# Kernel optimization log

Measured on AMD Instinct MI355X. Metric: run time of the kernel, lower is better.

The kernel has to match this reference:

```python
import jax, jax.numpy as jnp
import numpy as np

T, B, I, H = 256, 32, 128, 256
CLIP = 2.0

def setup_inputs() -> dict:
    key = jax.random.key(0)
    ks = jax.random.split(key, 10)
    si, sh = 1.0 / np.sqrt(I), 1.0 / np.sqrt(H)
    return {
        "x":     jax.random.normal(ks[0], (T, B, I), jnp.float32),
        "Wx":    jax.random.normal(ks[1], (4 * H, I), jnp.float32) * si,
        "bx":    jax.random.normal(ks[2], (4 * H,), jnp.float32) * si,
        "Wh":    jax.random.normal(ks[3], (4 * H, H), jnp.float32) * sh,
        "bh":    jax.random.normal(ks[4], (4 * H,), jnp.float32) * sh,
        "w_mod": jax.random.normal(ks[5], (1, H), jnp.float32) * sh,
        "b_mod": jax.random.normal(ks[6], (1,), jnp.float32) * sh,
        "w_fan": jax.random.normal(ks[7], (H, 1), jnp.float32),
        "b_fan": jax.random.normal(ks[8], (H,), jnp.float32),
        "alpha": 1e-4 * jax.random.uniform(ks[9], (H, H), jnp.float32),
    }

def reference(x, Wx, bx, Wh, bh, w_mod, b_mod, w_fan, b_fan, alpha):
    Bn = x.shape[1]
    # precompute input projection for all timesteps: [T, B, 4H]
    xf = jnp.einsum('tbi,gi->tbg', x, Wx) + bx

    def step(state, xf_t):
        h, c, hebb = state  # h,c: [B,H]; hebb: [B,H,H]
        fioj = xf_t + h @ Wh.T + bh                     # [B,4H]
        f = jax.nn.sigmoid(fioj[:, :H])
        i = jax.nn.sigmoid(fioj[:, H:2 * H])
        o = jax.nn.sigmoid(fioj[:, 2 * H:3 * H])
        # h_pred @ (alpha * hebb) : batched vec-mat product
        plast = jnp.einsum('bh,hk,bhk->bk', h, alpha, hebb)
        j = jnp.tanh(fioj[:, 3 * H:] + plast)
        c_new = f * c + i * j
        h_new = o * jnp.tanh(c_new)
        eta = jnp.tanh(c_new @ w_mod.T + b_mod)          # [B,1]
        myeta = eta * w_fan[:, 0] + b_fan                # [B,H] (Linear(1,H) fanout)
        # delta_hebb = outer(h_pred, j); eta modulates along the j axis
        hebb_new = jnp.clip(hebb + myeta[:, None, :] * (h[:, :, None] * j[:, None, :]),
                            -CLIP, CLIP)
        return (h_new, c_new, hebb_new), h_new

    init = (jnp.zeros((Bn, H), jnp.float32),
            jnp.zeros((Bn, H), jnp.float32),
            jnp.zeros((Bn, H, H), jnp.float32))
    (h, c, hebb), hs = jax.lax.scan(step, init, xf)
    return hs, h, c, hebb
```

## Files before the change

### kernel.cpp

```cpp
#include <hip/hip_runtime.h>


#define TT 256
#define BB 32
#define II 128
#define HH 256
#define G4 1024

typedef _Float16 h2_t __attribute__((ext_vector_type(2)));
typedef unsigned long long u64;

__device__ __forceinline__ float sigm(float x) {
    return 1.0f / (1.0f + __expf(-x));
}
__device__ __forceinline__ float tanhfast(float x) {
    return 1.0f - 2.0f / (__expf(2.0f * x) + 1.0f);
}
__device__ __forceinline__ unsigned pkh(float lo, float hi) {
    h2_t v;
    v.x = (_Float16)lo;
    v.y = (_Float16)hi;
    return __builtin_bit_cast(unsigned, v);
}

#if __has_builtin(__builtin_amdgcn_fdot2)
__device__ __forceinline__ float dot2(unsigned a, unsigned b, float c) {
    return __builtin_amdgcn_fdot2(__builtin_bit_cast(h2_t, a),
                                  __builtin_bit_cast(h2_t, b), c, false);
}
#else
__device__ __forceinline__ float dot2(unsigned a, unsigned b, float c) {
    h2_t av = __builtin_bit_cast(h2_t, a), bv = __builtin_bit_cast(h2_t, b);
    return c + (float)av.x * (float)bv.x + (float)av.y * (float)bv.y;
}
#endif

__device__ __forceinline__ h2_t pkfma(h2_t a, h2_t b, h2_t c) {
#if __has_builtin(__builtin_elementwise_fma)
    return __builtin_elementwise_fma(a, b, c);
#else
    return a * b + c;
#endif
}
__device__ __forceinline__ h2_t clip2h(h2_t x) {
    const h2_t lo = {(_Float16)-2.0f, (_Float16)-2.0f};
    const h2_t hi = {(_Float16)2.0f, (_Float16)2.0f};
#if __has_builtin(__builtin_elementwise_max) && __has_builtin(__builtin_elementwise_min)
    return __builtin_elementwise_min(__builtin_elementwise_max(x, lo), hi);
#else
    h2_t r = x;
    r.x = r.x < lo.x ? lo.x : (r.x > hi.x ? hi.x : r.x);
    r.y = r.y < lo.y ? lo.y : (r.y > hi.y ? hi.y : r.y);
    return r;
#endif
}

__device__ __forceinline__ void ld3_fast(const u64* p1, const u64* p2,
                                         const u64* p3,
                                         u64& v1, u64& v2, u64& v3) {
    asm volatile(
        "global_load_dwordx2 %0, %3, off sc0\n\t"
        "global_load_dwordx2 %1, %4, off sc0\n\t"
        "global_load_dwordx2 %2, %5, off sc0\n\t"
        "s_waitcnt vmcnt(0)"
        : "=&v"(v1), "=&v"(v2), "=&v"(v3)
        : "v"(p1), "v"(p2), "v"(p3));
}

__global__ __launch_bounds__(256) void prep_wd3(const float* __restrict__ Wh,
                                                uint4* __restrict__ Wd3) {
    int idx = blockIdx.x * 256 + threadIdx.x;
    int ro = idx >> 12, rem = idx & 4095;
    int g = rem >> 2, ri = rem & 3;
    int r8 = 4 * ro + ri;
    const float4* s = (const float4*)(Wh + (size_t)g * HH + (r8 << 3));
    float4 a = s[0], b2 = s[1];
    uint4 o;
    o.x = pkh(a.x, a.y);
    o.y = pkh(a.z, a.w);
    o.z = pkh(b2.x, b2.y);
    o.w = pkh(b2.z, b2.w);
    Wd3[idx] = o;
}

__global__ __launch_bounds__(256) void prep_alq(const float* __restrict__ alpha,
                                                uint4* __restrict__ alQ) {
    int idx = blockIdx.x * 256 + threadIdx.x;
    int p4 = idx >> 8, k = idx & 255;
    unsigned r[4];
#pragma unroll
    for (int j = 0; j < 4; ++j) {
        int p = 4 * p4 + j;
        float a0 = alpha[(size_t)(2 * p) * HH + k];
        float a1 = alpha[(size_t)(2 * p + 1) * HH + k];
        r[j] = pkh(a0, a1);
    }
    uint4 o; o.x = r[0]; o.y = r[1]; o.z = r[2]; o.w = r[3];
    alQ[idx] = o;
}

__global__ __launch_bounds__(256) void xf_gemm(const float* __restrict__ x,
                                               const float* __restrict__ Wx,
                                               const float* __restrict__ bx,
                                               const float* __restrict__ bh,
                                               float* __restrict__ xf) {
    __shared__ float As[64][37];
    __shared__ float Bs[64][37];
    const int tid = threadIdx.x;
    const int tx = tid & 15, ty = tid >> 4;
    const int m0 = blockIdx.y << 6;
    const int n0 = blockIdx.x << 6;
    float c[4][4] = {};

    for (int k0 = 0; k0 < II; k0 += 32) {
#pragma unroll
        for (int hh = 0; hh < 2; ++hh) {
            int row = (tid >> 3) + (hh << 5);
            int col = (tid & 7) << 2;
            float4 va = *(const float4*)(x + (size_t)(m0 + row) * II + k0 + col);
            As[row][col] = va.x; As[row][col + 1] = va.y;
            As[row][col + 2] = va.z; As[row][col + 3] = va.w;
            float4 vb = *(const float4*)(Wx + (size_t)(n0 + row) * II + k0 + col);
            Bs[row][col] = vb.x; Bs[row][col + 1] = vb.y;
            Bs[row][col + 2] = vb.z; Bs[row][col + 3] = vb.w;
        }
        __syncthreads();
#pragma unroll
        for (int kk = 0; kk < 32; ++kk) {
            float a[4], bb[4];
#pragma unroll
            for (int u = 0; u < 4; ++u) a[u] = As[(ty << 2) + u][kk];
#pragma unroll
            for (int v = 0; v < 4; ++v) bb[v] = Bs[(tx << 2) + v][kk];
#pragma unroll
            for (int u = 0; u < 4; ++u)
#pragma unroll
                for (int v = 0; v < 4; ++v)
                    c[u][v] = fmaf(a[u], bb[v], c[u][v]);
        }
        __syncthreads();
    }
    const int n = n0 + (tx << 2);
    float4 bxv = *(const float4*)(bx + n);
    float4 bhv = *(const float4*)(bh + n);
    float4 badd = {bxv.x + bhv.x, bxv.y + bhv.y, bxv.z + bhv.z, bxv.w + bhv.w};
#pragma unroll
    for (int u = 0; u < 4; ++u) {
        int m = m0 + (ty << 2) + u;
        float4 o = {c[u][0] + badd.x, c[u][1] + badd.y,
                    c[u][2] + badd.z, c[u][3] + badd.w};
        *(float4*)(xf + (size_t)m * G4 + n) = o;
    }
}

#define HBQ_FOREACH(X) X(0) X(1) X(2) X(3) X(4) X(5) X(6) X(7)

#define HBQ_DECL(i) h2_t hp##i = {(_Float16)0.0f, (_Float16)0.0f};
#define HBQ_OUT(i) \
    hbout[(size_t)(r0g + 2 * i) * HH + k]     = (float)hp##i.x; \
    hbout[(size_t)(r0g + 2 * i + 1) * HH + k] = (float)hp##i.y;

#define HBQ_STEP(i, au, hou, hnu) { \
    h2_t al2 = __builtin_bit_cast(h2_t, au); \
    h2_t ho2 = __builtin_bit_cast(h2_t, hou); \
    h2_t hn2 = __builtin_bit_cast(h2_t, hnu); \
    hp##i = clip2h(pkfma(mj2, ho2, hp##i)); \
    h2_t hna = hn2 * al2; \
    pp = dot2(__builtin_bit_cast(unsigned, hna), \
              __builtin_bit_cast(unsigned, hp##i), pp); }

#define HBQ_CHUNK(q, AV, i0, i1, i2, i3) { \
    uint4 ho = hfO4[hb4 + (q)]; \
    uint4 hn = hfN4[hb4 + (q)]; \
    HBQ_STEP(i0, AV.x, ho.x, hn.x) \
    HBQ_STEP(i1, AV.y, ho.y, hn.y) \
    HBQ_STEP(i2, AV.z, ho.z, hn.z) \
    HBQ_STEP(i3, AV.w, ho.w, hn.w) }

#define HBV_STEP(i, hou) { \
    h2_t ho2 = __builtin_bit_cast(h2_t, hou); \
    hp##i = clip2h(pkfma(mj2, ho2, hp##i)); }
#define HBV_CHUNK(q, i0, i1, i2, i3) { \
    uint4 ho = hfO4[hb4 + (q)]; \
    HBV_STEP(i0, ho.x) HBV_STEP(i1, ho.y) \
    HBV_STEP(i2, ho.z) HBV_STEP(i3, ho.w) }

#define DOTW(W, HV) { \
    ac0 = dot2(W.x, HV.x, ac0); ac1 = dot2(W.y, HV.y, ac1); \
    ac2 = dot2(W.z, HV.z, ac2); ac3 = dot2(W.w, HV.w, ac3); }

#define PUBLISH(val) { \
    u64 pkv = ((u64)tag << 32) | (u64)__builtin_bit_cast(unsigned, val); \
    __hip_atomic_store(&myF[off], pkv, __ATOMIC_RELAXED, \
                       __HIP_MEMORY_SCOPE_WORKGROUP); \
    __hip_atomic_store(&myEx[off], pkv, __ATOMIC_RELAXED, \
                       __HIP_MEMORY_SCOPE_AGENT); }

__global__ __launch_bounds__(1024, 1) void scan_kernel(
    const float* __restrict__ xf,
    const uint4* __restrict__ Wd3,
    const uint4* __restrict__ alQ,
    const float* __restrict__ w_mod,
    const float* __restrict__ b_mod,
    const float* __restrict__ w_fan,
    const float* __restrict__ b_fan,
    u64* __restrict__ exData,
    u64* __restrict__ exFast,
    float* __restrict__ out) {
    const int bid = blockIdx.x;
    const int r   = bid >> 5;
    const int b   = bid & 31;
    const int tid = threadIdx.x;
    const int k   = tid & (HH - 1);
    const int rg  = tid >> 8;
    const int r0g = r * 64 + rg * 16;
    const int hb4 = r0g >> 3;

    __shared__ alignas(16) unsigned short hf_s[2][HH];
    __shared__ float fioj_s[G4];
    __shared__ float pp_s[4][HH];
    __shared__ float red_s[4];

    HBQ_FOREACH(HBQ_DECL)

    if (tid < HH) {
        hf_s[0][tid] = 0;
        hf_s[1][tid] = 0;
    }
    if (tid < 4) red_s[tid] = 0.0f;
    __syncthreads();

    const float bmod = b_mod[0];
    const float wf = w_fan[k], bf = b_fan[k], wm = w_mod[k];
    float creg = 0.0f, jreg = 0.0f, hnreg = 0.0f;

    const uint4* wb = Wd3 + ((size_t)(2 * r) << 12) + (tid << 2);
    uint4 w0 = wb[0], w1 = wb[1], w2 = wb[2], w3 = wb[3];
    uint4 w4 = wb[4096], w5 = wb[4097], w6 = wb[4098], w7 = wb[4099];
    uint4 aqA = alQ[(size_t)(8 * r + 2 * rg) * 256 + k];
    uint4 aqB = alQ[(size_t)(8 * r + 2 * rg + 1) * 256 + k];

    const float* xfp = xf + (size_t)b * G4 + tid;
    float xcur = (rg == r) ? xfp[0] : 0.0f;

    u64* myEx = exData + (size_t)((b * 4 + r) * 2) * 1024;
    const u64* pEx1 = exData + (size_t)((b * 4 + ((r + 1) & 3)) * 2) * 1024;
    const u64* pEx2 = exData + (size_t)((b * 4 + ((r + 2) & 3)) * 2) * 1024;
    const u64* pEx3 = exData + (size_t)((b * 4 + ((r + 3) & 3)) * 2) * 1024;
    u64* myF = exFast + (size_t)((b * 4 + r) * 2) * 1024;
    const u64* pF1 = exFast + (size_t)((b * 4 + ((r + 1) & 3)) * 2) * 1024;
    const u64* pF2 = exFast + (size_t)((b * 4 + ((r + 2) & 3)) * 2) * 1024;
    const u64* pF3 = exFast + (size_t)((b * 4 + ((r + 3) & 3)) * 2) * 1024;

    for (int t = 0; t < TT; ++t) {
        float xnext = 0.0f;
        if (rg == r && t + 1 < TT) xnext = xfp[(size_t)(t + 1) * BB * G4];

        const unsigned tag = (unsigned)(t + 1);
        const int off = (t & 1) * 1024 + tid;

        float eta = tanhfast(((red_s[0] + red_s[1]) + (red_s[2] + red_s[3])) + bmod);
        float mj = fmaf(eta, wf, bf) * jreg;
        h2_t mj2;
        mj2.x = (_Float16)mj;
        mj2.y = mj2.x;
        const uint4* hfO4 = (const uint4*)hf_s[t & 1];
        const uint4* hfN4 = (const uint4*)hf_s[(t & 1) ^ 1];
        float pp = 0.0f;
        HBQ_CHUNK(0, aqA, 0, 1, 2, 3)
        HBQ_CHUNK(1, aqB, 4, 5, 6, 7)
        pp_s[rg][k] = pp;

        float ac0 = 0.f, ac1 = 0.f, ac2 = 0.f, ac3 = 0.f;
        {
            const int hx = r << 3;
            uint4 h0 = hfN4[hx], h1 = hfN4[hx + 1];
            uint4 h2 = hfN4[hx + 2], h3 = hfN4[hx + 3];
            DOTW(w0, h0) DOTW(w1, h1) DOTW(w2, h2) DOTW(w3, h3)
            uint4 h4 = hfN4[hx + 4], h5 = hfN4[hx + 5];
            uint4 h6 = hfN4[hx + 6], h7 = hfN4[hx + 7];
            DOTW(w4, h4) DOTW(w5, h5) DOTW(w6, h6) DOTW(w7, h7)
        }
        float part = ((ac0 + ac1) + (ac2 + ac3)) + xcur;
        xcur = xnext;

        if (tid < 768) PUBLISH(part)
        __syncthreads();

        if (tid >= 768) {
            int k2 = tid - 768;
            part += (pp_s[0][k2] + pp_s[1][k2]) + (pp_s[2][k2] + pp_s[3][k2]);
            PUBLISH(part)
        }

        {
            float s1 = 0.f, s2 = 0.f, s3 = 0.f;
            bool d1 = false, d2 = false, d3 = false;
            const u64* f1 = pF1 + off;
            const u64* f2 = pF2 + off;
            const u64* f3 = pF3 + off;
            int it = 0;
            do {
                u64 v1, v2, v3;
                if ((it & 3) != 3) {
                    ld3_fast(f1, f2, f3, v1, v2, v3);
                } else {
                    v1 = __hip_atomic_load(pEx1 + off, __ATOMIC_RELAXED,
                                           __HIP_MEMORY_SCOPE_AGENT);
                    v2 = __hip_atomic_load(pEx2 + off, __ATOMIC_RELAXED,
                                           __HIP_MEMORY_SCOPE_AGENT);
                    v3 = __hip_atomic_load(pEx3 + off, __ATOMIC_RELAXED,
                                           __HIP_MEMORY_SCOPE_AGENT);
                }
                ++it;
                if (!d1 && (unsigned)(v1 >> 32) == tag) {
                    s1 = __builtin_bit_cast(float, (unsigned)v1);
                    d1 = true;
                }
                if (!d2 && (unsigned)(v2 >> 32) == tag) {
                    s2 = __builtin_bit_cast(float, (unsigned)v2);
                    d2 = true;
                }
                if (!d3 && (unsigned)(v3 >> 32) == tag) {
                    s3 = __builtin_bit_cast(float, (unsigned)v3);
                    d3 = true;
                }
            } while (!(d1 && d2 && d3));
            fioj_s[tid] = part + ((s1 + s2) + s3);
        }
        __syncthreads();

        jreg = tanhfast(fioj_s[3 * HH + k]);
        if (rg == 0) {
            float fg = sigm(fioj_s[k]);
            float ig = sigm(fioj_s[HH + k]);
            float og = sigm(fioj_s[2 * HH + k]);
            creg = fmaf(fg, creg, ig * jreg);
            hnreg = og * tanhfast(creg);
            _Float16 hh = (_Float16)hnreg;
            hf_s[t & 1][k] = __builtin_bit_cast(unsigned short, hh);
            if (r == 0) out[((size_t)t * BB + b) * HH + k] = hnreg;
            float e = creg * wm;
#pragma unroll
            for (int m = 32; m >= 1; m >>= 1) e += __shfl_xor(e, m, 64);
            if ((k & 63) == 0) red_s[k >> 6] = e;
        }
        __syncthreads();
    }

    {
        float eta = tanhfast(((red_s[0] + red_s[1]) + (red_s[2] + red_s[3])) + bmod);
        float mj = fmaf(eta, wf, bf) * jreg;
        h2_t mj2;
        mj2.x = (_Float16)mj;
        mj2.y = mj2.x;
        const uint4* hfO4 = (const uint4*)hf_s[0];
        HBV_CHUNK(0, 0, 1, 2, 3)
        HBV_CHUNK(1, 4, 5, 6, 7)
    }

    const size_t HS = (size_t)TT * BB * HH;
    if (r == 0 && rg == 0) {
        out[HS + (size_t)b * HH + k]           = hnreg;
        out[HS + BB * HH + (size_t)b * HH + k] = creg;
    }
    float* hbout = out + HS + 2 * BB * HH + (size_t)b * HH * HH;
    HBQ_FOREACH(HBQ_OUT)
}

extern "C" void kernel_launch(void* const* d_in, const int* in_sizes, int n_in,
                              void* d_out, int out_size, void* d_ws,
                              size_t ws_size, hipStream_t stream) {
    const float* x     = (const float*)d_in[0];
    const float* Wx    = (const float*)d_in[1];
    const float* bx    = (const float*)d_in[2];
    const float* Wh    = (const float*)d_in[3];
    const float* bh    = (const float*)d_in[4];
    const float* w_mod = (const float*)d_in[5];
    const float* b_mod = (const float*)d_in[6];
    const float* w_fan = (const float*)d_in[7];
    const float* b_fan = (const float*)d_in[8];
    const float* alpha = (const float*)d_in[9];
    float* out = (float*)d_out;

    float* xf  = (float*)d_ws;
    uint4* Wd3 = (uint4*)((char*)d_ws + 33554432);
    uint4* alQ = (uint4*)((char*)d_ws + 34078720);
    u64*   exD = (u64*)((char*)d_ws + 34209792);
    u64*   exF = (u64*)((char*)d_ws + 36306944);

    hipLaunchKernelGGL(prep_wd3, dim3(128), dim3(256), 0, stream, Wh, Wd3);
    hipLaunchKernelGGL(prep_alq, dim3(32), dim3(256), 0, stream, alpha, alQ);
    hipLaunchKernelGGL(xf_gemm, dim3(16, 128), dim3(256), 0, stream,
                       x, Wx, bx, bh, xf);
    hipLaunchKernelGGL(scan_kernel, dim3(128), dim3(1024), 0, stream,
                       xf, Wd3, alQ, w_mod, b_mod, w_fan, b_fan,
                       exD, exF, out);
}
```

Before: 757.5 us.

## Remap threads so gate quads share a wavefront and drop one barrier per step

Threads are remapped so the four gates for one hidden unit sit in adjacent lanes. Gate activations and the plastic-term sum are exchanged with lane shuffles instead of shared-memory arrays, so every thread publishes its partial at once and one __syncthreads per timestep goes away. A triple-buffered h vector and double-buffered per-wave eta partials avoid read/write hazards without the second barrier. The cell-state update is now computed redundantly in all four lanes of each quad, and the x projection is split by 0.25 across all row groups, which changes the floating-point summation order.

```diff
diff --git a/kernel.cpp b/kernel.cpp
--- a/kernel.cpp
+++ b/kernel.cpp
@@ -169,9 +169,9 @@
     pp = dot2(__builtin_bit_cast(unsigned, hna), \
               __builtin_bit_cast(unsigned, hp##i), pp); }
 
-#define HBQ_CHUNK(q, AV, i0, i1, i2, i3) { \
-    uint4 ho = hfO4[hb4 + (q)]; \
-    uint4 hn = hfN4[hb4 + (q)]; \
+#define HBQ_CHUNK(cq, AV, i0, i1, i2, i3) { \
+    uint4 ho = hfO4[hb4 + (cq)]; \
+    uint4 hn = hfN4[hb4 + (cq)]; \
     HBQ_STEP(i0, AV.x, ho.x, hn.x) \
     HBQ_STEP(i1, AV.y, ho.y, hn.y) \
     HBQ_STEP(i2, AV.z, ho.z, hn.z) \
@@ -180,8 +180,8 @@
 #define HBV_STEP(i, hou) { \
     h2_t ho2 = __builtin_bit_cast(h2_t, hou); \
     hp##i = clip2h(pkfma(mj2, ho2, hp##i)); }
-#define HBV_CHUNK(q, i0, i1, i2, i3) { \
-    uint4 ho = hfO4[hb4 + (q)]; \
+#define HBV_CHUNK(cq, i0, i1, i2, i3) { \
+    uint4 ho = hfO4[hb4 + (cq)]; \
     HBV_STEP(i0, ho.x) HBV_STEP(i1, ho.y) \
     HBV_STEP(i2, ho.z) HBV_STEP(i3, ho.w) }
 
@@ -196,7 +196,15 @@
     __hip_atomic_store(&myEx[off], pkv, __ATOMIC_RELAXED, \
                        __HIP_MEMORY_SCOPE_AGENT); }
 
-__global__ __launch_bounds__(1024, 1) void scan_kernel(
+#define ETA_SUM(bank) ({ \
+    const float4* rp_ = (const float4*)red_s[bank]; \
+    float4 e0_ = rp_[0], e1_ = rp_[1], e2_ = rp_[2], e3_ = rp_[3]; \
+    (((e0_.x + e0_.y) + (e0_.z + e0_.w)) + \
+     ((e1_.x + e1_.y) + (e1_.z + e1_.w))) + \
+    (((e2_.x + e2_.y) + (e2_.z + e2_.w)) + \
+     ((e3_.x + e3_.y) + (e3_.z + e3_.w))); })
+
+__global__ __launch_bounds__(1024, 4) void scan_kernel(
     const float* __restrict__ xf,
     const uint4* __restrict__ Wd3,
     const uint4* __restrict__ alQ,
@@ -211,37 +219,35 @@
     const int r   = bid >> 5;
     const int b   = bid & 31;
     const int tid = threadIdx.x;
-    const int k   = tid & (HH - 1);
-    const int rg  = tid >> 8;
-    const int r0g = r * 64 + rg * 16;
+    const int wv  = tid >> 6;
+    const int l   = tid & 63;
+    const int q   = l & 3;
+    const int k   = (wv << 4) + (l >> 2);
+    const int g   = (q << 8) + k;
+    const int r0g = (r << 6) + (q << 4);
     const int hb4 = r0g >> 3;
 
-    __shared__ alignas(16) unsigned short hf_s[2][HH];
-    __shared__ float fioj_s[G4];
-    __shared__ float pp_s[4][HH];
-    __shared__ float red_s[4];
+    __shared__ alignas(16) unsigned short hf_s[3][HH];
+    __shared__ alignas(16) float red_s[2][16];
 
     HBQ_FOREACH(HBQ_DECL)
 
-    if (tid < HH) {
-        hf_s[0][tid] = 0;
-        hf_s[1][tid] = 0;
-    }
-    if (tid < 4) red_s[tid] = 0.0f;
+    if (tid < 3 * HH) ((unsigned short*)hf_s)[tid] = 0;
+    if (tid < 32) ((float*)red_s)[tid] = 0.0f;
     __syncthreads();
 
     const float bmod = b_mod[0];
     const float wf = w_fan[k], bf = b_fan[k], wm = w_mod[k];
     float creg = 0.0f, jreg = 0.0f, hnreg = 0.0f;
 
-    const uint4* wb = Wd3 + ((size_t)(2 * r) << 12) + (tid << 2);
+    const uint4* wb = Wd3 + ((size_t)(2 * r) << 12) + (g << 2);
     uint4 w0 = wb[0], w1 = wb[1], w2 = wb[2], w3 = wb[3];
     uint4 w4 = wb[4096], w5 = wb[4097], w6 = wb[4098], w7 = wb[4099];
-    uint4 aqA = alQ[(size_t)(8 * r + 2 * rg) * 256 + k];
-    uint4 aqB = alQ[(size_t)(8 * r + 2 * rg + 1) * 256 + k];
-
-    const float* xfp = xf + (size_t)b * G4 + tid;
-    float xcur = (rg == r) ? xfp[0] : 0.0f;
+    uint4 aqA = alQ[(size_t)(8 * r + 2 * q) * 256 + k];
+    uint4 aqB = alQ[(size_t)(8 * r + 2 * q + 1) * 256 + k];
+
+    const float* xfp = xf + (size_t)b * G4 + g;
+    float xcur = 0.25f * xfp[0];
 
     u64* myEx = exData + (size_t)((b * 4 + r) * 2) * 1024;
     const u64* pEx1 = exData + (size_t)((b * 4 + ((r + 1) & 3)) * 2) * 1024;
@@ -252,47 +258,44 @@
     const u64* pF2 = exFast + (size_t)((b * 4 + ((r + 2) & 3)) * 2) * 1024;
     const u64* pF3 = exFast + (size_t)((b * 4 + ((r + 3) & 3)) * 2) * 1024;
 
+    int iW = 0, iO = 1, iN = 2;
+
     for (int t = 0; t < TT; ++t) {
-        float xnext = 0.0f;
-        if (rg == r && t + 1 < TT) xnext = xfp[(size_t)(t + 1) * BB * G4];
+        float xnext = (t + 1 < TT) ? 0.25f * xfp[(size_t)(t + 1) * BB * G4]
+                                   : 0.0f;
 
         const unsigned tag = (unsigned)(t + 1);
-        const int off = (t & 1) * 1024 + tid;
-
-        float eta = tanhfast(((red_s[0] + red_s[1]) + (red_s[2] + red_s[3])) + bmod);
+        const int off = (t & 1) * 1024 + g;
+
+        const uint4* hfO4 = (const uint4*)hf_s[iO];
+        const uint4* hfN4 = (const uint4*)hf_s[iN];
+
+        float eta = tanhfast(ETA_SUM((t + 1) & 1) + bmod);
         float mj = fmaf(eta, wf, bf) * jreg;
         h2_t mj2;
         mj2.x = (_Float16)mj;
         mj2.y = mj2.x;
-        const uint4* hfO4 = (const uint4*)hf_s[t & 1];
-        const uint4* hfN4 = (const uint4*)hf_s[(t & 1) ^ 1];
         float pp = 0.0f;
         HBQ_CHUNK(0, aqA, 0, 1, 2, 3)
         HBQ_CHUNK(1, aqB, 4, 5, 6, 7)
-        pp_s[rg][k] = pp;
+        pp += __shfl_xor(pp, 1, 64);
+        pp += __shfl_xor(pp, 2, 64);
 
         float ac0 = 0.f, ac1 = 0.f, ac2 = 0.f, ac3 = 0.f;
         {
-            const int hx = r << 3;
-            uint4 h0 = hfN4[hx], h1 = hfN4[hx + 1];
-            uint4 h2 = hfN4[hx + 2], h3 = hfN4[hx + 3];
+            const uint4* hv = hfN4 + (r << 3);
+            uint4 h0 = hv[0], h1 = hv[1], h2 = hv[2], h3 = hv[3];
             DOTW(w0, h0) DOTW(w1, h1) DOTW(w2, h2) DOTW(w3, h3)
-            uint4 h4 = hfN4[hx + 4], h5 = hfN4[hx + 5];
-            uint4 h6 = hfN4[hx + 6], h7 = hfN4[hx + 7];
+            uint4 h4 = hv[4], h5 = hv[5], h6 = hv[6], h7 = hv[7];
             DOTW(w4, h4) DOTW(w5, h5) DOTW(w6, h6) DOTW(w7, h7)
         }
         float part = ((ac0 + ac1) + (ac2 + ac3)) + xcur;
         xcur = xnext;
-
-        if (tid < 768) PUBLISH(part)
-        __syncthreads();
-
-        if (tid >= 768) {
-            int k2 = tid - 768;
-            part += (pp_s[0][k2] + pp_s[1][k2]) + (pp_s[2][k2] + pp_s[3][k2]);
-            PUBLISH(part)
-        }
-
+        if (q == 3) part += pp;
+
+        PUBLISH(part)
+
+        float tot;
         {
             float s1 = 0.f, s2 = 0.f, s3 = 0.f;
             bool d1 = false, d2 = false, d3 = false;
@@ -326,41 +329,59 @@
                     d3 = true;
                 }
             } while (!(d1 && d2 && d3));
-            fioj_s[tid] = part + ((s1 + s2) + s3);
+            tot = part + ((s1 + s2) + s3);
         }
+
+        float scale = (q == 3) ? 2.0f : 1.0f;
+        float sg = 1.0f / (1.0f + __expf(-scale * tot));
+        float act = fmaf(sg, scale, (q == 3) ? -1.0f : 0.0f);
+
+        float x1v = __shfl_xor(act, 1, 64);
+        float x2v = __shfl_xor(act, 2, 64);
+        float x3v = __shfl_xor(x1v, 2, 64);
+        bool sA = (q & 1) != 0, sB = (q & 2) != 0;
+        float b0 = sA ? x1v : act;
+        float b1 = sA ? act : x1v;
+        float b2v = sA ? x3v : x2v;
+        float b3v = sA ? x2v : x3v;
+        float fg = sB ? b2v : b0;
+        float og = sB ? b0 : b2v;
+        float ig = sB ? b3v : b1;
+        float jg = sB ? b1 : b3v;
+
+        jreg = jg;
+        creg = fmaf(fg, creg, ig * jg);
+        hnreg = og * tanhfast(creg);
+        if (q == 0) {
+            _Float16 hh = (_Float16)hnreg;
+            hf_s[iW][k] = __builtin_bit_cast(unsigned short, hh);
+            if (r == 0) out[((size_t)t * BB + b) * HH + k] = hnreg;
+        }
+        float e = creg * wm;
+        e += __shfl_xor(e, 4, 64);
+        e += __shfl_xor(e, 8, 64);
+        e += __shfl_xor(e, 16, 64);
+        e += __shfl_xor(e, 32, 64);
+        if (l == 0) red_s[t & 1][wv] = e;
+
         __syncthreads();
 
-        jreg = tanhfast(fioj_s[3 * HH + k]);
-        if (rg == 0) {
-            float fg = sigm(fioj_s[k]);
-            float ig = sigm(fioj_s[HH + k]);
-            float og = sigm(fioj_s[2 * HH + k]);
-            creg = fmaf(fg, creg, ig * jreg);
-            hnreg = og * tanhfast(creg);
-            _Float16 hh = (_Float16)hnreg;
-            hf_s[t & 1][k] = __builtin_bit_cast(unsigned short, hh);
-            if (r == 0) out[((size_t)t * BB + b) * HH + k] = hnreg;
-            float e = creg * wm;
-#pragma unroll
-            for (int m = 32; m >= 1; m >>= 1) e += __shfl_xor(e, m, 64);
-            if ((k & 63) == 0) red_s[k >> 6] = e;
-        }
-        __syncthreads();
+        int tmp = iW; iW = iO; iO = iN; iN = tmp;
     }
 
     {
-        float eta = tanhfast(((red_s[0] + red_s[1]) + (red_s[2] + red_s[3])) + bmod);
+        float eta = tanhfast(ETA_SUM(1) + bmod);
         float mj = fmaf(eta, wf, bf) * jreg;
         h2_t mj2;
         mj2.x = (_Float16)mj;
         mj2.y = mj2.x;
-        const uint4* hfO4 = (const uint4*)hf_s[0];
+        const uint4* hfO4 = (const uint4*)hf_s[2];
         HBV_CHUNK(0, 0, 1, 2, 3)
         HBV_CHUNK(1, 4, 5, 6, 7)
     }
 
     const size_t HS = (size_t)TT * BB * HH;
-    if (r == 0 && rg == 0) {
+    if (r == 0 && q == 0) {
         out[HS + (size_t)b * HH + k]           = hnreg;
         out[HS + BB * HH + (size_t)b * HH + k] = creg;
     }
```

New measurement: 1.515 ms. +100.0%, slower.

## Remap hebb ownership to quads and exchange plastic partials separately

Applied to the files above, without the earlier changes.

Hebbian rows are remapped so that each group of four adjacent threads covers one column k, with the partial plasticity sums reduced by shuffles instead of a shared-memory array. All 1024 threads now publish their gate partial right away, without waiting on a barrier to fold in the plastic term. The plastic partials go through a separate exchange buffer, and the j-gate threads poll both buffers together. This removes a serialized publish phase from the per-step critical path, at the cost of extra polling traffic and a strided hebb output write pattern.

```diff
diff --git a/kernel.cpp b/kernel.cpp
--- a/kernel.cpp
+++ b/kernel.cpp
@@ -65,6 +65,22 @@
         "s_waitcnt vmcnt(0)"
         : "=&v"(v1), "=&v"(v2), "=&v"(v3)
         : "v"(p1), "v"(p2), "v"(p3));
+}
+__device__ __forceinline__ void ld6_fast(const u64* p1, const u64* p2,
+                                         const u64* p3, const u64* p4,
+                                         const u64* p5, const u64* p6,
+                                         u64& v1, u64& v2, u64& v3,
+                                         u64& v4, u64& v5, u64& v6) {
+    asm volatile(
+        "global_load_dwordx2 %0, %6, off sc0\n\t"
+        "global_load_dwordx2 %1, %7, off sc0\n\t"
+        "global_load_dwordx2 %2, %8, off sc0\n\t"
+        "global_load_dwordx2 %3, %9, off sc0\n\t"
+        "global_load_dwordx2 %4, %10, off sc0\n\t"
+        "global_load_dwordx2 %5, %11, off sc0\n\t"
+        "s_waitcnt vmcnt(0)"
+        : "=&v"(v1), "=&v"(v2), "=&v"(v3), "=&v"(v4), "=&v"(v5), "=&v"(v6)
+        : "v"(p1), "v"(p2), "v"(p3), "v"(p4), "v"(p5), "v"(p6));
 }
 
 __global__ __launch_bounds__(256) void prep_wd3(const float* __restrict__ Wh,
@@ -157,8 +173,8 @@
 
 #define HBQ_DECL(i) h2_t hp##i = {(_Float16)0.0f, (_Float16)0.0f};
 #define HBQ_OUT(i) \
-    hbout[(size_t)(r0g + 2 * i) * HH + k]     = (float)hp##i.x; \
-    hbout[(size_t)(r0g + 2 * i + 1) * HH + k] = (float)hp##i.y;
+    hbout[(size_t)(r0g + 2 * i) * HH + kq]     = (float)hp##i.x; \
+    hbout[(size_t)(r0g + 2 * i + 1) * HH + kq] = (float)hp##i.y;
 
 #define HBQ_STEP(i, au, hou, hnu) { \
     h2_t al2 = __builtin_bit_cast(h2_t, au); \
@@ -169,9 +185,9 @@
     pp = dot2(__builtin_bit_cast(unsigned, hna), \
               __builtin_bit_cast(unsigned, hp##i), pp); }
 
-#define HBQ_CHUNK(q, AV, i0, i1, i2, i3) { \
-    uint4 ho = hfO4[hb4 + (q)]; \
-    uint4 hn = hfN4[hb4 + (q)]; \
+#define HBQ_CHUNK(cq, AV, i0, i1, i2, i3) { \
+    uint4 ho = hfO4[hb4 + (cq)]; \
+    uint4 hn = hfN4[hb4 + (cq)]; \
     HBQ_STEP(i0, AV.x, ho.x, hn.x) \
     HBQ_STEP(i1, AV.y, ho.y, hn.y) \
     HBQ_STEP(i2, AV.z, ho.z, hn.z) \
@@ -180,8 +196,8 @@
 #define HBV_STEP(i, hou) { \
     h2_t ho2 = __builtin_bit_cast(h2_t, hou); \
     hp##i = clip2h(pkfma(mj2, ho2, hp##i)); }
-#define HBV_CHUNK(q, i0, i1, i2, i3) { \
-    uint4 ho = hfO4[hb4 + (q)]; \
+#define HBV_CHUNK(cq, i0, i1, i2, i3) { \
+    uint4 ho = hfO4[hb4 + (cq)]; \
     HBV_STEP(i0, ho.x) HBV_STEP(i1, ho.y) \
     HBV_STEP(i2, ho.z) HBV_STEP(i3, ho.w) }
 
@@ -194,6 +210,13 @@
     __hip_atomic_store(&myF[off], pkv, __ATOMIC_RELAXED, \
                        __HIP_MEMORY_SCOPE_WORKGROUP); \
     __hip_atomic_store(&myEx[off], pkv, __ATOMIC_RELAXED, \
+                       __HIP_MEMORY_SCOPE_AGENT); }
+
+#define PUBPP(val) { \
+    u64 pkv = ((u64)tag << 32) | (u64)__builtin_bit_cast(unsigned, val); \
+    __hip_atomic_store(&myPPf[ppo + kq], pkv, __ATOMIC_RELAXED, \
+                       __HIP_MEMORY_SCOPE_WORKGROUP); \
+    __hip_atomic_store(&myPPd[ppo + kq], pkv, __ATOMIC_RELAXED, \
                        __HIP_MEMORY_SCOPE_AGENT); }
 
 __global__ __launch_bounds__(1024, 1) void scan_kernel(
@@ -206,6 +229,8 @@
     const float* __restrict__ b_fan,
     u64* __restrict__ exData,
     u64* __restrict__ exFast,
+    u64* __restrict__ ppData,
+    u64* __restrict__ ppFast,
     float* __restrict__ out) {
     const int bid = blockIdx.x;
     const int r   = bid >> 5;
@@ -213,12 +238,14 @@
     const int tid = threadIdx.x;
     const int k   = tid & (HH - 1);
     const int rg  = tid >> 8;
-    const int r0g = r * 64 + rg * 16;
+    const int q   = tid & 3;
+    const int kq  = tid >> 2;
+    const int r0g = (r << 6) + (q << 4);
     const int hb4 = r0g >> 3;
 
     __shared__ alignas(16) unsigned short hf_s[2][HH];
     __shared__ float fioj_s[G4];
-    __shared__ float pp_s[4][HH];
+    __shared__ float pp_s[HH];
     __shared__ float red_s[4];
 
     HBQ_FOREACH(HBQ_DECL)
@@ -231,14 +258,16 @@
     __syncthreads();
 
     const float bmod = b_mod[0];
-    const float wf = w_fan[k], bf = b_fan[k], wm = w_mod[k];
-    float creg = 0.0f, jreg = 0.0f, hnreg = 0.0f;
+    const float wfq = w_fan[kq], bfq = b_fan[kq];
+    const float wm = w_mod[k];
+    float creg = 0.0f, hnreg = 0.0f;
+    float jq = 0.0f;
 
     const uint4* wb = Wd3 + ((size_t)(2 * r) << 12) + (tid << 2);
     uint4 w0 = wb[0], w1 = wb[1], w2 = wb[2], w3 = wb[3];
     uint4 w4 = wb[4096], w5 = wb[4097], w6 = wb[4098], w7 = wb[4099];
-    uint4 aqA = alQ[(size_t)(8 * r + 2 * rg) * 256 + k];
-    uint4 aqB = alQ[(size_t)(8 * r + 2 * rg + 1) * 256 + k];
+    uint4 aqA = alQ[(size_t)(8 * r + 2 * q) * 256 + kq];
+    uint4 aqB = alQ[(size_t)(8 * r + 2 * q + 1) * 256 + kq];
 
     const float* xfp = xf + (size_t)b * G4 + tid;
     float xcur = (rg == r) ? xfp[0] : 0.0f;
@@ -251,6 +280,14 @@
     const u64* pF1 = exFast + (size_t)((b * 4 + ((r + 1) & 3)) * 2) * 1024;
     const u64* pF2 = exFast + (size_t)((b * 4 + ((r + 2) & 3)) * 2) * 1024;
     const u64* pF3 = exFast + (size_t)((b * 4 + ((r + 3) & 3)) * 2) * 1024;
+    u64* myPPd = ppData + (size_t)((b * 4 + r) * 2) * 256;
+    u64* myPPf = ppFast + (size_t)((b * 4 + r) * 2) * 256;
+    const u64* pPd1 = ppData + (size_t)((b * 4 + ((r + 1) & 3)) * 2) * 256;
+    const u64* pPd2 = ppData + (size_t)((b * 4 + ((r + 2) & 3)) * 2) * 256;
+    const u64* pPd3 = ppData + (size_t)((b * 4 + ((r + 3) & 3)) * 2) * 256;
+    const u64* pPf1 = ppFast + (size_t)((b * 4 + ((r + 1) & 3)) * 2) * 256;
+    const u64* pPf2 = ppFast + (size_t)((b * 4 + ((r + 2) & 3)) * 2) * 256;
+    const u64* pPf3 = ppFast + (size_t)((b * 4 + ((r + 3) & 3)) * 2) * 256;
 
     for (int t = 0; t < TT; ++t) {
         float xnext = 0.0f;
@@ -258,9 +295,10 @@
 
         const unsigned tag = (unsigned)(t + 1);
         const int off = (t & 1) * 1024 + tid;
+        const int ppo = (t & 1) * 256;
 
         float eta = tanhfast(((red_s[0] + red_s[1]) + (red_s[2] + red_s[3])) + bmod);
-        float mj = fmaf(eta, wf, bf) * jreg;
+        float mj = fmaf(eta, wfq, bfq) * jq;
         h2_t mj2;
         mj2.x = (_Float16)mj;
         mj2.y = mj2.x;
@@ -269,7 +307,12 @@
         float pp = 0.0f;
         HBQ_CHUNK(0, aqA, 0, 1, 2, 3)
         HBQ_CHUNK(1, aqB, 4, 5, 6, 7)
-        pp_s[rg][k] = pp;
+        pp += __shfl_xor(pp, 1, 64);
+        pp += __shfl_xor(pp, 2, 64);
+        if (q == 0) {
+            pp_s[kq] = pp;
+            PUBPP(pp)
+        }
 
         float ac0 = 0.f, ac1 = 0.f, ac2 = 0.f, ac3 = 0.f;
         {
@@ -284,16 +327,11 @@
         float part = ((ac0 + ac1) + (ac2 + ac3)) + xcur;
         xcur = xnext;
 
-        if (tid < 768) PUBLISH(part)
+        PUBLISH(part)
         __syncthreads();
 
-        if (tid >= 768) {
-            int k2 = tid - 768;
-            part += (pp_s[0][k2] + pp_s[1][k2]) + (pp_s[2][k2] + pp_s[3][k2]);
-            PUBLISH(part)
-        }
-
-        {
+        float fv;
+        if (tid < 768) {
             float s1 = 0.f, s2 = 0.f, s3 = 0.f;
             bool d1 = false, d2 = false, d3 = false;
             const u64* f1 = pF1 + off;
@@ -326,16 +364,78 @@
                     d3 = true;
                 }
             } while (!(d1 && d2 && d3));
-            fioj_s[tid] = part + ((s1 + s2) + s3);
+            fv = part + ((s1 + s2) + s3);
+        } else {
+            const int k2 = tid - 768;
+            const int po = ppo + k2;
+            float own = pp_s[k2];
+            float s1 = 0.f, s2 = 0.f, s3 = 0.f;
+            float u1 = 0.f, u2 = 0.f, u3 = 0.f;
+            bool d1 = false, d2 = false, d3 = false;
+            bool e1 = false, e2 = false, e3 = false;
+            const u64* f1 = pF1 + off;
+            const u64* f2 = pF2 + off;
+            const u64* f3 = pF3 + off;
+            const u64* g1 = pPf1 + po;
+            const u64* g2 = pPf2 + po;
+            const u64* g3 = pPf3 + po;
+            int it = 0;
+            do {
+                u64 v1, v2, v3, y1, y2, y3;
+                if ((it & 3) != 3) {
+                    ld6_fast(f1, f2, f3, g1, g2, g3, v1, v2, v3, y1, y2, y3);
+                } else {
+                    v1 = __hip_atomic_load(pEx1 + off, __ATOMIC_RELAXED,
+                                           __HIP_MEMORY_SCOPE_AGENT);
+                    v2 = __hip_atomic_load(pEx2 + off, __ATOMIC_RELAXED,
+                                           __HIP_MEMORY_SCOPE_AGENT);
+                    v3 = __hip_atomic_load(pEx3 + off, __ATOMIC_RELAXED,
+                                           __HIP_MEMORY_SCOPE_AGENT);
+                    y1 = __hip_atomic_load(pPd1 + po, __ATOMIC_RELAXED,
+                                           __HIP_MEMORY_SCOPE_AGENT);
+                    y2 = __hip_atomic_load(pPd2 + po, __ATOMIC_RELAXED,
+                                           __HIP_MEMORY_SCOPE_AGENT);
+                    y3 = __hip_atomic_load(pPd3 + po, __ATOMIC_RELAXED,
+                                           __HIP_MEMORY_SCOPE_AGENT);
+                }
+                ++it;
+                if (!d1 && (unsigned)(v1 >> 32) == tag) {
+                    s1 = __builtin_bit_cast(float, (unsigned)v1);
+                    d1 = true;
+                }
+                if (!d2 && (unsigned)(v2 >> 32) == tag) {
+                    s2 = __builtin_bit_cast(float, (unsigned)v2);
+                    d2 = true;
+                }
+                if (!d3 && (unsigned)(v3 >> 32) == tag) {
+                    s3 = __builtin_bit_cast(float, (unsigned)v3);
+                    d3 = true;
+                }
+                if (!e1 && (unsigned)(y1 >> 32) == tag) {
+                    u1 = __builtin_bit_cast(float, (unsigned)y1);
+                    e1 = true;
+                }
+                if (!e2 && (unsigned)(y2 >> 32) == tag) {
+                    u2 = __builtin_bit_cast(float, (unsigned)y2);
+                    e2 = true;
+                }
+                if (!e3 && (unsigned)(y3 >> 32) == tag) {
+                    u3 = __builtin_bit_cast(float, (unsigned)y3);
+                    e3 = true;
+                }
+            } while (!(d1 && d2 && d3 && e1 && e2 && e3));
+            fv = ((part + own) + ((s1 + s2) + s3)) + ((u1 + u2) + u3);
         }
+        fioj_s[tid] = fv;
         __syncthreads();
 
-        jreg = tanhfast(fioj_s[3 * HH + k]);
+        jq = tanhfast(fioj_s[3 * HH + kq]);
         if (rg == 0) {
             float fg = sigm(fioj_s[k]);
             float ig = sigm(fioj_s[HH + k]);
             float og = sigm(fioj_s[2 * HH + k]);
-            creg = fmaf(fg, creg, ig * jreg);
+            float jk = tanhfast(fioj_s[3 * HH + k]);
+            creg = fmaf(fg, creg, ig * jk);
             hnreg = og * tanhfast(creg);
             _Float16 hh = (_Float16)hnreg;
             hf_s[t & 1][k] = __builtin_bit_cast(unsigned short, hh);
@@ -350,7 +450,7 @@
 
     {
         float eta = tanhfast(((red_s[0] + red_s[1]) + (red_s[2] + red_s[3])) + bmod);
-        float mj = fmaf(eta, wf, bf) * jreg;
+        float mj = fmaf(eta, wfq, bfq) * jq;
         h2_t mj2;
         mj2.x = (_Float16)mj;
         mj2.y = mj2.x;
@@ -388,6 +488,8 @@
     uint4* alQ = (uint4*)((char*)d_ws + 34078720);
     u64*   exD = (u64*)((char*)d_ws + 34209792);
     u64*   exF = (u64*)((char*)d_ws + 36306944);
+    u64*   ppD = (u64*)((char*)d_ws + 38404096);
+    u64*   ppF = (u64*)((char*)d_ws + 38928384);
 
     hipLaunchKernelGGL(prep_wd3, dim3(128), dim3(256), 0, stream, Wh, Wd3);
     hipLaunchKernelGGL(prep_alq, dim3(32), dim3(256), 0, stream, alpha, alQ);
@@ -395,5 +497,5 @@
                        x, Wx, bx, bh, xf);
     hipLaunchKernelGGL(scan_kernel, dim3(128), dim3(1024), 0, stream,
                        xf, Wd3, alQ, w_mod, b_mod, w_fan, b_fan,
-                       exD, exF, out);
-}
+                       exD, exF, ppD, ppF, out);
+}
```

Result: slower. 866.8 us (+14.4%).
